# Kernel tuning notes

Hardware: AMD Instinct MI355X
Metric: run time of the kernel (lower is better)

The kernel has to match this reference:

```python
import jax, jax.numpy as jnp
import numpy as np

B, H, IN, T = 32768, 128, 128, 10
SPARSITY = 0.8


def setup_inputs() -> dict:
    key = jax.random.key(0)
    ks = jax.random.split(key, 12)
    x = jax.random.normal(ks[0], (B, IN), dtype=jnp.float32)
    hidden = jax.random.normal(ks[1], (B, H), dtype=jnp.float32)
    time_span = jnp.linspace(0.0, 1.0, T).astype(jnp.float32)
    # sparse binary wiring mask: rand < 1 - sparsity (WiringType.ADAPTIVE default branch)
    wiring = (jax.random.uniform(ks[2], (H, H)) < (1.0 - SPARSITY)).astype(jnp.float32)
    W = jax.random.normal(ks[3], (H, H), dtype=jnp.float32) * 0.1
    b = jnp.zeros((H,), dtype=jnp.float32)
    W_in = jax.random.normal(ks[4], (H, IN), dtype=jnp.float32) / np.sqrt(IN)
    b_in = jnp.zeros((H,), dtype=jnp.float32)
    W_upd = jax.random.normal(ks[5], (H, H + IN), dtype=jnp.float32) / np.sqrt(H + IN)
    b_upd = jnp.zeros((H,), dtype=jnp.float32)
    W_rst = jax.random.normal(ks[6], (H, H + IN), dtype=jnp.float32) / np.sqrt(H + IN)
    b_rst = jnp.zeros((H,), dtype=jnp.float32)
    return dict(x=x, hidden=hidden, time_span=time_span, wiring=wiring, W=W, b=b,
                W_in=W_in, b_in=b_in, W_upd=W_upd, b_upd=b_upd, W_rst=W_rst, b_rst=b_rst)


def reference(x, hidden, time_span, wiring, W, b, W_in, b_in, W_upd, b_upd, W_rst, b_rst):
    # input projection and GRU-style gates on [hidden, x]
    x_proj = x @ W_in.T + b_in                                   # [B, H]
    combined = jnp.concatenate([hidden, x], axis=1)              # [B, H+IN]
    update = jax.nn.sigmoid(combined @ W_upd.T + b_upd)          # [B, H]
    reset = jax.nn.sigmoid(combined @ W_rst.T + b_rst)           # [B, H]
    h0 = reset * hidden                                          # [B, H]

    W_eff_T = (W * wiring).T                                     # [H, H], masked recurrent weights

    def f(h):
        # dh/dt = -h + tanh(W_eff h + b) + x_proj  (tau = 1.0: config has no log_tau attr)
        return -h + jnp.tanh(h @ W_eff_T + b) + x_proj

    def rk4_step(h, dt):
        k1 = f(h)
        k2 = f(h + 0.5 * dt * k1)
        k3 = f(h + 0.5 * dt * k2)
        k4 = f(h + dt * k3)
        h_new = h + (dt / 6.0) * (k1 + 2.0 * k2 + 2.0 * k3 + k4)
        return h_new, h_new

    dts = jnp.diff(time_span)                                    # [T-1]
    h_last, traj = jax.lax.scan(rk4_step, h0, dts)               # traj: [T-1, B, H]
    ode_out = jnp.concatenate([h0[None], traj], axis=0)          # [T, B, H]
    new_hidden = update * h_last + (1.0 - update) * h0           # [B, H]
    return new_hidden, ode_out
```

## Files before the change

### kernel.cpp

```cpp
#include <hip/hip_runtime.h>


constexpr int kB   = 32768;
constexpr int kH   = 128;
constexpr int kIn  = 128;
constexpr int kT   = 10;
constexpr int ROWS = 64;
constexpr int LDSW = 136;
constexpr int HIN  = 256;

typedef __bf16 bf16;
typedef __attribute__((ext_vector_type(8))) __bf16 bf16x8;
typedef __attribute__((ext_vector_type(4))) __bf16 bf16x4;
typedef __attribute__((ext_vector_type(4))) float  f32x4;

__device__ __forceinline__ float sigmoid_(float v) {
  return __fdividef(1.0f, 1.0f + __expf(-v));
}
__device__ __forceinline__ float tanh_(float v) {
  float a = fabsf(v);
  float e = __expf(-2.0f * a);
  float r = __fdividef(1.0f - e, 1.0f + e);
  return v < 0.0f ? -r : r;
}

__device__ __forceinline__ bf16x8 cvt8(const float* p) {
  float4 f0 = *(const float4*)p;
  float4 f1 = *(const float4*)(p + 4);
  bf16x8 t;
  t[0]=(bf16)f0.x; t[1]=(bf16)f0.y; t[2]=(bf16)f0.z; t[3]=(bf16)f0.w;
  t[4]=(bf16)f1.x; t[5]=(bf16)f1.y; t[6]=(bf16)f1.z; t[7]=(bf16)f1.w;
  return t;
}

__device__ __forceinline__ void gemm4(
    f32x4 (&C)[2][4], const bf16 (*S)[LDSW],
    const float* __restrict__ Wb, int ldw, int kofs,
    int wave, int quad, int l16)
{
#pragma unroll
  for (int kk = 0; kk < 4; ++kk) {
    bf16x8 af[2];
#pragma unroll
    for (int a = 0; a < 2; ++a)
      af[a] = cvt8(Wb + (size_t)((wave*2 + a)*16 + l16) * ldw + kofs + kk*32 + quad*8);
#pragma unroll
    for (int nt = 0; nt < 4; ++nt) {
      bf16x8 bfv = *(const bf16x8*)&S[nt*16 + l16][kk*32 + quad*8];
#pragma unroll
      for (int a = 0; a < 2; ++a)
        C[a][nt] = __builtin_amdgcn_mfma_f32_16x16x32_bf16(af[a], bfv, C[a][nt], 0, 0, 0);
    }
  }
}

__device__ __forceinline__ void feval(
    f32x4 (&K)[2][4], const bf16x8 (&weff)[2][4], const bf16 (*Y)[LDSW],
    float4 bv0, float4 bv1, int quad, int l16)
{
#pragma unroll
  for (int nt = 0; nt < 4; ++nt) {
    K[0][nt] = f32x4{bv0.x, bv0.y, bv0.z, bv0.w};
    K[1][nt] = f32x4{bv1.x, bv1.y, bv1.z, bv1.w};
  }
#pragma unroll
  for (int kk = 0; kk < 4; ++kk)
#pragma unroll
    for (int nt = 0; nt < 4; ++nt) {
      bf16x8 bfv = *(const bf16x8*)&Y[nt*16 + l16][kk*32 + quad*8];
#pragma unroll
      for (int a = 0; a < 2; ++a)
        K[a][nt] = __builtin_amdgcn_mfma_f32_16x16x32_bf16(weff[a][kk], bfv, K[a][nt], 0, 0, 0);
    }
}

__device__ __forceinline__ void storeTile(
    bf16 (*Y)[LDSW], float* gbase, const f32x4 (&V)[2][4], int hc0, int l16)
{
#pragma unroll
  for (int a = 0; a < 2; ++a)
#pragma unroll
    for (int nt = 0; nt < 4; ++nt) {
      bf16x4 p;
      p[0]=(bf16)V[a][nt][0]; p[1]=(bf16)V[a][nt][1];
      p[2]=(bf16)V[a][nt][2]; p[3]=(bf16)V[a][nt][3];
      int r = nt*16 + l16;
      *(bf16x4*)&Y[r][hc0 + a*16] = p;
      if (gbase) {
        float4 g{V[a][nt][0], V[a][nt][1], V[a][nt][2], V[a][nt][3]};
        *(float4*)(gbase + (size_t)r * kH + hc0 + a*16) = g;
      }
    }
}

__global__ __launch_bounds__(256, 2) void ltc_kernel(
    const float* __restrict__ x,     const float* __restrict__ hidden,
    const float* __restrict__ ts,    const float* __restrict__ wiring,
    const float* __restrict__ W,     const float* __restrict__ bb_,
    const float* __restrict__ W_in,  const float* __restrict__ b_in,
    const float* __restrict__ W_upd, const float* __restrict__ b_upd,
    const float* __restrict__ W_rst, const float* __restrict__ b_rst,
    float* __restrict__ out)
{
  __shared__ bf16 ldsX [ROWS][LDSW];
  __shared__ bf16 ldsHd[ROWS][LDSW];
  __shared__ bf16 ldsY [ROWS][LDSW];
  __shared__ float sts[kT];

  const int tid  = threadIdx.x;
  const int wave = tid >> 6;
  const int lane = tid & 63;
  const int quad = lane >> 4;
  const int l16  = lane & 15;
  const int r0   = blockIdx.x * ROWS;

  if (tid < kT) sts[tid] = ts[tid];

#pragma unroll
  for (int i = 0; i < 8; ++i) {
    int idx = i*256 + tid;
    int row = idx >> 5;
    int c4  = (idx & 31) * 4;
    float4 vx = *(const float4*)(x      + (size_t)(r0+row)*kIn + c4);
    float4 vh = *(const float4*)(hidden + (size_t)(r0+row)*kH  + c4);
    bf16x4 bx; bx[0]=(bf16)vx.x; bx[1]=(bf16)vx.y; bx[2]=(bf16)vx.z; bx[3]=(bf16)vx.w;
    bf16x4 bh; bh[0]=(bf16)vh.x; bh[1]=(bf16)vh.y; bh[2]=(bf16)vh.z; bh[3]=(bf16)vh.w;
    *(bf16x4*)&ldsX [row][c4] = bx;
    *(bf16x4*)&ldsHd[row][c4] = bh;
  }

  const int hc0 = wave*32 + quad*4;

  bf16x8 weff[2][4];
#pragma unroll
  for (int a = 0; a < 2; ++a) {
    int hrow = (wave*2 + a)*16 + l16;
#pragma unroll
    for (int kk = 0; kk < 4; ++kk) {
      int k = kk*32 + quad*8;
      const float* wp = W      + (size_t)hrow*kH + k;
      const float* mp = wiring + (size_t)hrow*kH + k;
      float4 w0 = *(const float4*)wp, w1 = *(const float4*)(wp+4);
      float4 m0 = *(const float4*)mp, m1 = *(const float4*)(mp+4);
      bf16x8 t;
      t[0]=(bf16)(w0.x*m0.x); t[1]=(bf16)(w0.y*m0.y);
      t[2]=(bf16)(w0.z*m0.z); t[3]=(bf16)(w0.w*m0.w);
      t[4]=(bf16)(w1.x*m1.x); t[5]=(bf16)(w1.y*m1.y);
      t[6]=(bf16)(w1.z*m1.z); t[7]=(bf16)(w1.w*m1.w);
      weff[a][kk] = t;
    }
  }
  float4 bv0 = *(const float4*)(bb_ + hc0);
  float4 bv1 = *(const float4*)(bb_ + hc0 + 16);

  __syncthreads();

  f32x4 xp[2][4];
  {
    float4 bi0 = *(const float4*)(b_in + hc0);
    float4 bi1 = *(const float4*)(b_in + hc0 + 16);
#pragma unroll
    for (int nt = 0; nt < 4; ++nt) {
      xp[0][nt] = f32x4{bi0.x, bi0.y, bi0.z, bi0.w};
      xp[1][nt] = f32x4{bi1.x, bi1.y, bi1.z, bi1.w};
    }
    gemm4(xp, ldsX, W_in, kIn, 0, wave, quad, l16);
  }

  f32x4 h[2][4], U[2][4];
  {
    f32x4 R[2][4];
    float4 br0 = *(const float4*)(b_rst + hc0);
    float4 br1 = *(const float4*)(b_rst + hc0 + 16);
    float4 bu0 = *(const float4*)(b_upd + hc0);
    float4 bu1 = *(const float4*)(b_upd + hc0 + 16);
#pragma unroll
    for (int nt = 0; nt < 4; ++nt) {
      R[0][nt] = f32x4{br0.x, br0.y, br0.z, br0.w};
      R[1][nt] = f32x4{br1.x, br1.y, br1.z, br1.w};
      U[0][nt] = f32x4{bu0.x, bu0.y, bu0.z, bu0.w};
      U[1][nt] = f32x4{bu1.x, bu1.y, bu1.z, bu1.w};
    }
    gemm4(R, ldsHd, W_rst, HIN, 0,  wave, quad, l16);
    gemm4(R, ldsX,  W_rst, HIN, kH, wave, quad, l16);
    gemm4(U, ldsHd, W_upd, HIN, 0,  wave, quad, l16);
    gemm4(U, ldsX,  W_upd, HIN, kH, wave, quad, l16);

#pragma unroll
    for (int a = 0; a < 2; ++a)
#pragma unroll
      for (int nt = 0; nt < 4; ++nt) {
        const float* hp = hidden + (size_t)(r0 + nt*16 + l16)*kH + hc0 + a*16;
        float4 hv = *(const float4*)hp;
        h[a][nt][0] = sigmoid_(R[a][nt][0]) * hv.x;
        h[a][nt][1] = sigmoid_(R[a][nt][1]) * hv.y;
        h[a][nt][2] = sigmoid_(R[a][nt][2]) * hv.z;
        h[a][nt][3] = sigmoid_(R[a][nt][3]) * hv.w;
        U[a][nt][0] = sigmoid_(U[a][nt][0]);
        U[a][nt][1] = sigmoid_(U[a][nt][1]);
        U[a][nt][2] = sigmoid_(U[a][nt][2]);
        U[a][nt][3] = sigmoid_(U[a][nt][3]);
      }
  }

  __syncthreads();

  storeTile(ldsHd, nullptr, U, hc0, l16);
  float* ode0 = out + (size_t)kB*kH + (size_t)r0*kH;
  storeTile(ldsX,  nullptr, h, hc0, l16);
  storeTile(ldsY,  ode0,    h, hc0, l16);

  f32x4 z[2][4], hacc[2][4], K[2][4];
#pragma unroll
  for (int a = 0; a < 2; ++a)
#pragma unroll
    for (int nt = 0; nt < 4; ++nt) z[a][nt] = h[a][nt];

  for (int t = 1; t < kT; ++t) {
    float dt  = sts[t] - sts[t-1];
    float dt6 = dt * (1.0f/6.0f);
    float dt3 = dt * (1.0f/3.0f);
    float dth = 0.5f * dt;

    __syncthreads(); feval(K, weff, ldsY, bv0, bv1, quad, l16); __syncthreads();
#pragma unroll
    for (int a = 0; a < 2; ++a)
#pragma unroll
      for (int nt = 0; nt < 4; ++nt)
#pragma unroll
        for (int i = 0; i < 4; ++i) {
          float kv = tanh_(K[a][nt][i]) + xp[a][nt][i] - z[a][nt][i];
          hacc[a][nt][i] = h[a][nt][i] + dt6 * kv;
          z[a][nt][i]    = h[a][nt][i] + dth * kv;
        }
    storeTile(ldsY, nullptr, z, hc0, l16);

    __syncthreads(); feval(K, weff, ldsY, bv0, bv1, quad, l16); __syncthreads();
#pragma unroll
    for (int a = 0; a < 2; ++a)
#pragma unroll
      for (int nt = 0; nt < 4; ++nt)
#pragma unroll
        for (int i = 0; i < 4; ++i) {
          float kv = tanh_(K[a][nt][i]) + xp[a][nt][i] - z[a][nt][i];
          hacc[a][nt][i] += dt3 * kv;
          z[a][nt][i]     = h[a][nt][i] + dth * kv;
        }
    storeTile(ldsY, nullptr, z, hc0, l16);

    __syncthreads(); feval(K, weff, ldsY, bv0, bv1, quad, l16); __syncthreads();
#pragma unroll
    for (int a = 0; a < 2; ++a)
#pragma unroll
      for (int nt = 0; nt < 4; ++nt)
#pragma unroll
        for (int i = 0; i < 4; ++i) {
          float kv = tanh_(K[a][nt][i]) + xp[a][nt][i] - z[a][nt][i];
          hacc[a][nt][i] += dt3 * kv;
          z[a][nt][i]     = h[a][nt][i] + dt * kv;
        }
    storeTile(ldsY, nullptr, z, hc0, l16);

    __syncthreads(); feval(K, weff, ldsY, bv0, bv1, quad, l16); __syncthreads();
#pragma unroll
    for (int a = 0; a < 2; ++a)
#pragma unroll
      for (int nt = 0; nt < 4; ++nt)
#pragma unroll
        for (int i = 0; i < 4; ++i) {
          float kv = tanh_(K[a][nt][i]) + xp[a][nt][i] - z[a][nt][i];
          h[a][nt][i] = hacc[a][nt][i] + dt6 * kv;
          z[a][nt][i] = h[a][nt][i];
        }
    float* odet = out + (size_t)kB*kH + ((size_t)t*kB + r0)*kH;
    storeTile(ldsY, odet, h, hc0, l16);
  }

#pragma unroll
  for (int a = 0; a < 2; ++a)
#pragma unroll
    for (int nt = 0; nt < 4; ++nt) {
      int r = nt*16 + l16;
      bf16x4 uv  = *(const bf16x4*)&ldsHd[r][hc0 + a*16];
      bf16x4 h0v = *(const bf16x4*)&ldsX [r][hc0 + a*16];
      float4 p;
      {
        float uu;
        uu = (float)uv[0]; p.x = uu * h[a][nt][0] + (1.0f - uu) * (float)h0v[0];
        uu = (float)uv[1]; p.y = uu * h[a][nt][1] + (1.0f - uu) * (float)h0v[1];
        uu = (float)uv[2]; p.z = uu * h[a][nt][2] + (1.0f - uu) * (float)h0v[2];
        uu = (float)uv[3]; p.w = uu * h[a][nt][3] + (1.0f - uu) * (float)h0v[3];
      }
      *(float4*)(out + (size_t)(r0 + r) * kH + hc0 + a*16) = p;
    }
}

extern "C" void kernel_launch(void* const* d_in, const int* in_sizes, int n_in,
                              void* d_out, int out_size, void* d_ws, size_t ws_size,
                              hipStream_t stream) {
  (void)d_ws; (void)ws_size; (void)out_size;
  int ix=0, ih=1, its=2, iwr=3, iW=4, ib=5, iWin=6, ibin=7, iWu=8, ibu=9, iWr=10, ibr=11;
  if (n_in == 12 && in_sizes[2] != 10 && in_sizes[5] == 10) {
    ib=0; ibin=1; ibr=2; ibu=3; ih=4; its=5; iW=6; iWin=7; iWr=8; iWu=9; iwr=10; ix=11;
  }
  const float* x      = (const float*)d_in[ix];
  const float* hidden = (const float*)d_in[ih];
  const float* ts     = (const float*)d_in[its];
  const float* wiring = (const float*)d_in[iwr];
  const float* W      = (const float*)d_in[iW];
  const float* b      = (const float*)d_in[ib];
  const float* W_in   = (const float*)d_in[iWin];
  const float* b_in   = (const float*)d_in[ibin];
  const float* W_upd  = (const float*)d_in[iWu];
  const float* b_upd  = (const float*)d_in[ibu];
  const float* W_rst  = (const float*)d_in[iWr];
  const float* b_rst  = (const float*)d_in[ibr];

  dim3 grid(kB / ROWS);
  dim3 block(256);
  ltc_kernel<<<grid, block, 0, stream>>>(x, hidden, ts, wiring, W, b,
                                         W_in, b_in, W_upd, b_upd, W_rst, b_rst,
                                         (float*)d_out);
}
```

Baseline: 355.1 us.

## Halve rows per block, double-buffer LDS stage tiles, drop redundant barriers

Cuts rows per block from 64 to 32 and raises the launch-bounds occupancy hint from 2 to 4 blocks per CU. Ping-pongs the RK4 stage vectors between two LDS buffers, so each stage needs one __syncthreads instead of two. The global trajectory store is deferred and issued alongside the next feval, and tanh is replaced by a cheaper branchless exp formula. The costs are more blocks, each redoing the weight loads and conversions, and possible overflow or precision issues in the new tanh for large inputs.

```diff
diff --git a/kernel.cpp b/kernel.cpp
--- a/kernel.cpp
+++ b/kernel.cpp
@@ -5,7 +5,8 @@
 constexpr int kH   = 128;
 constexpr int kIn  = 128;
 constexpr int kT   = 10;
-constexpr int ROWS = 64;
+constexpr int ROWS = 32;
+constexpr int NT   = ROWS / 16;
 constexpr int LDSW = 136;
 constexpr int HIN  = 256;
 
@@ -18,10 +19,8 @@
   return __fdividef(1.0f, 1.0f + __expf(-v));
 }
 __device__ __forceinline__ float tanh_(float v) {
-  float a = fabsf(v);
-  float e = __expf(-2.0f * a);
-  float r = __fdividef(1.0f - e, 1.0f + e);
-  return v < 0.0f ? -r : r;
+  float e = __expf(2.0f * v);
+  return 1.0f - __fdividef(2.0f, 1.0f + e);
 }
 
 __device__ __forceinline__ bf16x8 cvt8(const float* p) {
@@ -34,7 +33,7 @@
 }
 
 __device__ __forceinline__ void gemm4(
-    f32x4 (&C)[2][4], const bf16 (*S)[LDSW],
+    f32x4 (&C)[2][NT], const bf16 (*S)[LDSW],
     const float* __restrict__ Wb, int ldw, int kofs,
     int wave, int quad, int l16)
 {
@@ -45,7 +44,7 @@
     for (int a = 0; a < 2; ++a)
       af[a] = cvt8(Wb + (size_t)((wave*2 + a)*16 + l16) * ldw + kofs + kk*32 + quad*8);
 #pragma unroll
-    for (int nt = 0; nt < 4; ++nt) {
+    for (int nt = 0; nt < NT; ++nt) {
       bf16x8 bfv = *(const bf16x8*)&S[nt*16 + l16][kk*32 + quad*8];
 #pragma unroll
       for (int a = 0; a < 2; ++a)
@@ -55,18 +54,18 @@
 }
 
 __device__ __forceinline__ void feval(
-    f32x4 (&K)[2][4], const bf16x8 (&weff)[2][4], const bf16 (*Y)[LDSW],
+    f32x4 (&K)[2][NT], const bf16x8 (&weff)[2][4], const bf16 (*Y)[LDSW],
     float4 bv0, float4 bv1, int quad, int l16)
 {
 #pragma unroll
-  for (int nt = 0; nt < 4; ++nt) {
+  for (int nt = 0; nt < NT; ++nt) {
     K[0][nt] = f32x4{bv0.x, bv0.y, bv0.z, bv0.w};
     K[1][nt] = f32x4{bv1.x, bv1.y, bv1.z, bv1.w};
   }
 #pragma unroll
   for (int kk = 0; kk < 4; ++kk)
 #pragma unroll
-    for (int nt = 0; nt < 4; ++nt) {
+    for (int nt = 0; nt < NT; ++nt) {
       bf16x8 bfv = *(const bf16x8*)&Y[nt*16 + l16][kk*32 + quad*8];
 #pragma unroll
       for (int a = 0; a < 2; ++a)
@@ -75,25 +74,32 @@
 }
 
 __device__ __forceinline__ void storeTile(
-    bf16 (*Y)[LDSW], float* gbase, const f32x4 (&V)[2][4], int hc0, int l16)
+    bf16 (*Y)[LDSW], const f32x4 (&V)[2][NT], int hc0, int l16)
 {
 #pragma unroll
   for (int a = 0; a < 2; ++a)
 #pragma unroll
-    for (int nt = 0; nt < 4; ++nt) {
+    for (int nt = 0; nt < NT; ++nt) {
       bf16x4 p;
       p[0]=(bf16)V[a][nt][0]; p[1]=(bf16)V[a][nt][1];
       p[2]=(bf16)V[a][nt][2]; p[3]=(bf16)V[a][nt][3];
-      int r = nt*16 + l16;
-      *(bf16x4*)&Y[r][hc0 + a*16] = p;
-      if (gbase) {
-        float4 g{V[a][nt][0], V[a][nt][1], V[a][nt][2], V[a][nt][3]};
-        *(float4*)(gbase + (size_t)r * kH + hc0 + a*16) = g;
-      }
-    }
-}
-
-__global__ __launch_bounds__(256, 2) void ltc_kernel(
+      *(bf16x4*)&Y[nt*16 + l16][hc0 + a*16] = p;
+    }
+}
+
+__device__ __forceinline__ void storeGlob(
+    float* gbase, const f32x4 (&V)[2][NT], int hc0, int l16)
+{
+#pragma unroll
+  for (int a = 0; a < 2; ++a)
+#pragma unroll
+    for (int nt = 0; nt < NT; ++nt) {
+      float4 g{V[a][nt][0], V[a][nt][1], V[a][nt][2], V[a][nt][3]};
+      *(float4*)(gbase + (size_t)(nt*16 + l16) * kH + hc0 + a*16) = g;
+    }
+}
+
+__global__ __launch_bounds__(256, 4) void ltc_kernel(
     const float* __restrict__ x,     const float* __restrict__ hidden,
     const float* __restrict__ ts,    const float* __restrict__ wiring,
     const float* __restrict__ W,     const float* __restrict__ bb_,
@@ -104,7 +110,8 @@
 {
   __shared__ bf16 ldsX [ROWS][LDSW];
   __shared__ bf16 ldsHd[ROWS][LDSW];
-  __shared__ bf16 ldsY [ROWS][LDSW];
+  __shared__ bf16 ldsY0[ROWS][LDSW];
+  __shared__ bf16 ldsY1[ROWS][LDSW];
   __shared__ float sts[kT];
 
   const int tid  = threadIdx.x;
@@ -117,7 +124,7 @@
   if (tid < kT) sts[tid] = ts[tid];
 
 #pragma unroll
-  for (int i = 0; i < 8; ++i) {
+  for (int i = 0; i < 4; ++i) {
     int idx = i*256 + tid;
     int row = idx >> 5;
     int c4  = (idx & 31) * 4;
@@ -155,27 +162,27 @@
 
   __syncthreads();
 
-  f32x4 xp[2][4];
+  f32x4 xp[2][NT];
   {
     float4 bi0 = *(const float4*)(b_in + hc0);
     float4 bi1 = *(const float4*)(b_in + hc0 + 16);
 #pragma unroll
-    for (int nt = 0; nt < 4; ++nt) {
+    for (int nt = 0; nt < NT; ++nt) {
       xp[0][nt] = f32x4{bi0.x, bi0.y, bi0.z, bi0.w};
       xp[1][nt] = f32x4{bi1.x, bi1.y, bi1.z, bi1.w};
     }
     gemm4(xp, ldsX, W_in, kIn, 0, wave, quad, l16);
   }
 
-  f32x4 h[2][4], U[2][4];
+  f32x4 h[2][NT], U[2][NT];
   {
-    f32x4 R[2][4];
+    f32x4 R[2][NT];
     float4 br0 = *(const float4*)(b_rst + hc0);
     float4 br1 = *(const float4*)(b_rst + hc0 + 16);
     float4 bu0 = *(const float4*)(b_upd + hc0);
     float4 bu1 = *(const float4*)(b_upd + hc0 + 16);
 #pragma unroll
-    for (int nt = 0; nt < 4; ++nt) {
+    for (int nt = 0; nt < NT; ++nt) {
       R[0][nt] = f32x4{br0.x, br0.y, br0.z, br0.w};
       R[1][nt] = f32x4{br1.x, br1.y, br1.z, br1.w};
       U[0][nt] = f32x4{bu0.x, bu0.y, bu0.z, bu0.w};
@@ -189,7 +196,7 @@
 #pragma unroll
     for (int a = 0; a < 2; ++a)
 #pragma unroll
-      for (int nt = 0; nt < 4; ++nt) {
+      for (int nt = 0; nt < NT; ++nt) {
         const float* hp = hidden + (size_t)(r0 + nt*16 + l16)*kH + hc0 + a*16;
         float4 hv = *(const float4*)hp;
         h[a][nt][0] = sigmoid_(R[a][nt][0]) * hv.x;
@@ -205,16 +212,17 @@
 
   __syncthreads();
 
-  storeTile(ldsHd, nullptr, U, hc0, l16);
-  float* ode0 = out + (size_t)kB*kH + (size_t)r0*kH;
-  storeTile(ldsX,  nullptr, h, hc0, l16);
-  storeTile(ldsY,  ode0,    h, hc0, l16);
-
-  f32x4 z[2][4], hacc[2][4], K[2][4];
+  storeTile(ldsHd, U, hc0, l16);
+  storeTile(ldsX,  h, hc0, l16);
+  storeTile(ldsY0, h, hc0, l16);
+
+  f32x4 z[2][NT], hacc[2][NT], K[2][NT];
 #pragma unroll
   for (int a = 0; a < 2; ++a)
 #pragma unroll
-    for (int nt = 0; nt < 4; ++nt) z[a][nt] = h[a][nt];
+    for (int nt = 0; nt < NT; ++nt) z[a][nt] = h[a][nt];
+
+  float* odeBase = out + (size_t)kB*kH + (size_t)r0*kH;
 
   for (int t = 1; t < kT; ++t) {
     float dt  = sts[t] - sts[t-1];
@@ -222,64 +230,70 @@
     float dt3 = dt * (1.0f/3.0f);
     float dth = 0.5f * dt;
 
-    __syncthreads(); feval(K, weff, ldsY, bv0, bv1, quad, l16); __syncthreads();
-#pragma unroll
-    for (int a = 0; a < 2; ++a)
-#pragma unroll
-      for (int nt = 0; nt < 4; ++nt)
+    __syncthreads();
+    storeGlob(odeBase + (size_t)(t-1)*kB*kH, h, hc0, l16);
+    feval(K, weff, ldsY0, bv0, bv1, quad, l16);
+#pragma unroll
+    for (int a = 0; a < 2; ++a)
+#pragma unroll
+      for (int nt = 0; nt < NT; ++nt)
 #pragma unroll
         for (int i = 0; i < 4; ++i) {
           float kv = tanh_(K[a][nt][i]) + xp[a][nt][i] - z[a][nt][i];
           hacc[a][nt][i] = h[a][nt][i] + dt6 * kv;
           z[a][nt][i]    = h[a][nt][i] + dth * kv;
         }
-    storeTile(ldsY, nullptr, z, hc0, l16);
-
-    __syncthreads(); feval(K, weff, ldsY, bv0, bv1, quad, l16); __syncthreads();
-#pragma unroll
-    for (int a = 0; a < 2; ++a)
-#pragma unroll
-      for (int nt = 0; nt < 4; ++nt)
+    storeTile(ldsY1, z, hc0, l16);
+
+    __syncthreads();
+    feval(K, weff, ldsY1, bv0, bv1, quad, l16);
+#pragma unroll
+    for (int a = 0; a < 2; ++a)
+#pragma unroll
+      for (int nt = 0; nt < NT; ++nt)
 #pragma unroll
         for (int i = 0; i < 4; ++i) {
           float kv = tanh_(K[a][nt][i]) + xp[a][nt][i] - z[a][nt][i];
           hacc[a][nt][i] += dt3 * kv;
           z[a][nt][i]     = h[a][nt][i] + dth * kv;
         }
-    storeTile(ldsY, nullptr, z, hc0, l16);
-
-    __syncthreads(); feval(K, weff, ldsY, bv0, bv1, quad, l16); __syncthreads();
-#pragma unroll
-    for (int a = 0; a < 2; ++a)
-#pragma unroll
-      for (int nt = 0; nt < 4; ++nt)
+    storeTile(ldsY0, z, hc0, l16);
+
+    __syncthreads();
+    feval(K, weff, ldsY0, bv0, bv1, quad, l16);
+#pragma unroll
+    for (int a = 0; a < 2; ++a)
+#pragma unroll
+      for (int nt = 0; nt < NT; ++nt)
 #pragma unroll
         for (int i = 0; i < 4; ++i) {
           float kv = tanh_(K[a][nt][i]) + xp[a][nt][i] - z[a][nt][i];
           hacc[a][nt][i] += dt3 * kv;
           z[a][nt][i]     = h[a][nt][i] + dt * kv;
         }
-    storeTile(ldsY, nullptr, z, hc0, l16);
-
-    __syncthreads(); feval(K, weff, ldsY, bv0, bv1, quad, l16); __syncthreads();
-#pragma unroll
-    for (int a = 0; a < 2; ++a)
-#pragma unroll
-      for (int nt = 0; nt < 4; ++nt)
+    storeTile(ldsY1, z, hc0, l16);
+
+    __syncthreads();
+    feval(K, weff, ldsY1, bv0, bv1, quad, l16);
+#pragma unroll
+    for (int a = 0; a < 2; ++a)
+#pragma unroll
+      for (int nt = 0; nt < NT; ++nt)
 #pragma unroll
         for (int i = 0; i < 4; ++i) {
           float kv = tanh_(K[a][nt][i]) + xp[a][nt][i] - z[a][nt][i];
           h[a][nt][i] = hacc[a][nt][i] + dt6 * kv;
           z[a][nt][i] = h[a][nt][i];
         }
-    float* odet = out + (size_t)kB*kH + ((size_t)t*kB + r0)*kH;
-    storeTile(ldsY, odet, h, hc0, l16);
-  }
+    storeTile(ldsY0, z, hc0, l16);
+  }
+
+  storeGlob(odeBase + (size_t)(kT-1)*kB*kH, h, hc0, l16);
 
 #pragma unroll
   for (int a = 0; a < 2; ++a)
 #pragma unroll
-    for (int nt = 0; nt < 4; ++nt) {
+    for (int nt = 0; nt < NT; ++nt) {
       int r = nt*16 + l16;
       bf16x4 uv  = *(const bf16x4*)&ldsHd[r][hc0 + a*16];
       bf16x4 h0v = *(const bf16x4*)&ldsX [r][hc0 + a*16];
```

Measured after the change: 421.1 us. 1.19x slower.
